# Kernel optimization log

Hardware: AMD Instinct MI355X
Metric: run time of the kernel (lower is better)

Reference implementation:

```python
import jax, jax.numpy as jnp
import numpy as np

D = 1024  # input_dim

def setup_inputs() -> dict:
    key = jax.random.key(0)
    ks = jax.random.split(key, 7)
    s = 1.0 / np.sqrt(D)
    x = jax.random.normal(ks[0], (8, 2048, D), dtype=jnp.float32)
    Wq = jax.random.uniform(ks[1], (D, D), jnp.float32, -s, s)
    bq = jax.random.uniform(ks[2], (D,), jnp.float32, -s, s)
    Wk = jax.random.uniform(ks[3], (D, D), jnp.float32, -s, s)
    bk = jax.random.uniform(ks[4], (D,), jnp.float32, -s, s)
    Wv = jax.random.uniform(ks[5], (D, D), jnp.float32, -s, s)
    bv = jax.random.uniform(ks[6], (D,), jnp.float32, -s, s)
    return {"x": x, "Wq": Wq, "bq": bq, "Wk": Wk, "bk": bk, "Wv": Wv, "bv": bv}

def reference(x, Wq, bq, Wk, bk, Wv, bv):
    # torch.nn.Linear: y = x @ W.T + b
    q = jnp.einsum('bsd,ed->bse', x, Wq) + bq
    k = jnp.einsum('bsd,ed->bse', x, Wk) + bk
    v = jnp.einsum('bsd,ed->bse', x, Wv) + bv
    scores = jnp.einsum('bqd,bkd->bqk', q, k) / jnp.sqrt(jnp.float32(x.shape[-1]))
    attn = jax.nn.softmax(scores, axis=2)
    return jnp.einsum('bqk,bkd->bqd', attn, v)
```

## Files before the change

### kernel.cpp

```cpp
#include <hip/hip_runtime.h>
#include <stdint.h>


typedef __bf16 bf16_t;
typedef __bf16 bf16x8 __attribute__((ext_vector_type(8)));
typedef __bf16 bf16x4 __attribute__((ext_vector_type(4)));
typedef float f32x4 __attribute__((ext_vector_type(4)));

__device__ __forceinline__ void gload_lds16(const bf16_t* g, bf16_t* l) {
    __builtin_amdgcn_global_load_lds((const __attribute__((address_space(1))) void*)g,
                                     (__attribute__((address_space(3))) void*)l,
                                     16, 0, 0);
}

template <int EPI, int LDA, int LDB>
__device__ __forceinline__ void gemm256_core(
    bf16_t* __restrict__ lds,
    const bf16_t* __restrict__ A,
    const bf16_t* __restrict__ B,
    bf16_t* __restrict__ Cb, float* __restrict__ Cf, int ldc,
    float* __restrict__ aux, float scale, int K,
    int m0, int n0)
{
    const int t    = threadIdx.x;
    const int lane = t & 63;
    const int wave = t >> 6;
    const int wm   = wave >> 2;
    const int wn   = wave & 3;
    const int lr   = lane & 15;
    const int quad = lane >> 4;

    const int rowS = t >> 2;
    const int qS   = (t & 3) ^ ((rowS >> 1) & 3);
    const bf16_t* Ag = A + (size_t)(m0 + rowS) * LDA + qS * 8;
    const bf16_t* Bg = B + (size_t)(n0 + rowS) * LDB + qS * 8;
    const int dst0 = t * 8;

    const int ko   = (quad ^ ((lr >> 1) & 3)) * 8;
    const int aoff = (wm * 128 + lr) * 32 + ko;
    const int boff = (wn * 64 + lr) * 32 + ko;

    f32x4 acc[8][4];
#pragma unroll
    for (int i = 0; i < 8; i++)
#pragma unroll
        for (int j = 0; j < 4; j++) acc[i][j] = (f32x4){0.f, 0.f, 0.f, 0.f};

    const int T = K >> 5;

#pragma unroll
    for (int tt = 0; tt < 3; ++tt) {
        bf16_t* Ab = lds + tt * 16384;
        bf16_t* Bb = Ab + 8192;
        const int kt = tt * 32;
        gload_lds16(Ag + kt,                     Ab + dst0);
        gload_lds16(Ag + kt + (size_t)128 * LDA, Ab + 4096 + dst0);
        gload_lds16(Bg + kt,                     Bb + dst0);
        gload_lds16(Bg + kt + (size_t)128 * LDB, Bb + 4096 + dst0);
    }
    asm volatile("s_waitcnt vmcnt(8)" ::: "memory");
    __builtin_amdgcn_s_barrier();
    __builtin_amdgcn_sched_barrier(0);

    for (int tk = 0; tk < T; ++tk) {
        const bf16_t* Ab = lds + (tk & 3) * 16384;
        const bf16_t* Bb = Ab + 8192;
        bf16x8 af[8], bfr[4];
#pragma unroll
        for (int j = 0; j < 4; ++j)
            bfr[j] = *(const bf16x8*)(Bb + boff + 512 * j);
#pragma unroll
        for (int i = 0; i < 8; ++i)
            af[i] = *(const bf16x8*)(Ab + aoff + 512 * i);
        __builtin_amdgcn_s_barrier();
        __builtin_amdgcn_sched_barrier(0);
        __builtin_amdgcn_s_setprio(1);
#pragma unroll
        for (int i = 0; i < 4; ++i)
#pragma unroll
            for (int j = 0; j < 4; ++j)
                acc[i][j] = __builtin_amdgcn_mfma_f32_16x16x32_bf16(af[i], bfr[j], acc[i][j], 0, 0, 0);
        __builtin_amdgcn_s_setprio(0);
        if (tk + 3 < T) {
            bf16_t* An = lds + ((tk + 3) & 3) * 16384;
            bf16_t* Bn = An + 8192;
            const int kt = (tk + 3) * 32;
            gload_lds16(Ag + kt,                     An + dst0);
            gload_lds16(Ag + kt + (size_t)128 * LDA, An + 4096 + dst0);
            gload_lds16(Bg + kt,                     Bn + dst0);
            gload_lds16(Bg + kt + (size_t)128 * LDB, Bn + 4096 + dst0);
            asm volatile("s_waitcnt vmcnt(8)" ::: "memory");
        } else if (tk + 2 < T) {
            asm volatile("s_waitcnt vmcnt(4)" ::: "memory");
        } else {
            asm volatile("s_waitcnt vmcnt(0)" ::: "memory");
        }
        __builtin_amdgcn_s_barrier();
        __builtin_amdgcn_sched_barrier(0);
        __builtin_amdgcn_s_setprio(1);
#pragma unroll
        for (int i = 4; i < 8; ++i)
#pragma unroll
            for (int j = 0; j < 4; ++j)
                acc[i][j] = __builtin_amdgcn_mfma_f32_16x16x32_bf16(af[i], bfr[j], acc[i][j], 0, 0, 0);
        __builtin_amdgcn_s_setprio(0);
    }

    if (EPI == 0 || EPI == 1) {
#pragma unroll
        for (int h = 0; h < 2; ++h) {
            __syncthreads();
            if (wm == h) {
#pragma unroll
                for (int j = 0; j < 4; ++j) {
                    const int col = wn * 64 + j * 16 + lr;
                    const float bv = (EPI == 0) ? aux[n0 + col] : 0.f;
#pragma unroll
                    for (int i = 0; i < 8; ++i) {
                        const int row = i * 16 + quad * 4;
#pragma unroll
                        for (int r = 0; r < 4; ++r) {
                            float v = (EPI == 0) ? (acc[i][j][r] + bv)
                                                 : __expf(acc[i][j][r] * scale);
                            lds[(row + r) * 264 + col] = (__bf16)v;
                        }
                    }
                }
            }
            __syncthreads();
            const int r2 = t >> 2;
            const int c0 = (t & 3) * 8;
            float part = 0.f;
#pragma unroll
            for (int c = 0; c < 8; ++c) {
                bf16x8 v = *(const bf16x8*)(lds + r2 * 264 + c0 + c * 32);
                *(bf16x8*)(Cb + (size_t)(m0 + h * 128 + r2) * ldc + n0 + c0 + c * 32) = v;
                if (EPI == 1) {
#pragma unroll
                    for (int e = 0; e < 8; ++e) part += (float)v[e];
                }
            }
            if (EPI == 1) {
                part += __shfl_xor(part, 1);
                part += __shfl_xor(part, 2);
                if ((t & 3) == 0) atomicAdd(aux + m0 + h * 128 + r2, part);
            }
        }
    } else if (EPI == 2) {
#pragma unroll
        for (int j = 0; j < 4; ++j) {
            const int col = n0 + wn * 64 + j * 16 + lr;
            const float s = 1.0f / aux[col];
            float* ccol = Cf + (size_t)col * ldc + m0 + wm * 128;
#pragma unroll
            for (int i = 0; i < 8; ++i) {
                f32x4 v = acc[i][j];
                v[0] *= s; v[1] *= s; v[2] *= s; v[3] *= s;
                *(f32x4*)(ccol + i * 16 + quad * 4) = v;
            }
        }
    } else {
#pragma unroll
        for (int j = 0; j < 4; ++j) {
            const int col = n0 + wn * 64 + j * 16 + lr;
            const float bv = aux[col];
#pragma unroll
            for (int i = 0; i < 8; ++i) {
                const int rowg = m0 + wm * 128 + i * 16 + quad * 4;
                const int b    = rowg >> 11;
                const int s    = rowg & 2047;
                bf16x4 p = { (__bf16)(acc[i][j][0] + bv), (__bf16)(acc[i][j][1] + bv),
                             (__bf16)(acc[i][j][2] + bv), (__bf16)(acc[i][j][3] + bv) };
                *(bf16x4*)(Cb + ((size_t)b << 21) + ((size_t)col << 11) + s) = p;
            }
        }
    }
}


__global__ __launch_bounds__(512, 1) void k_qkv3(
    const bf16_t* __restrict__ xb, const bf16_t* __restrict__ Wb,
    bf16_t* __restrict__ Q, bf16_t* __restrict__ Vt,
    const float* __restrict__ bq, const float* __restrict__ bk,
    const float* __restrict__ bv)
{
    __shared__ bf16_t lds[65536];
    const int lid  = blockIdx.x + 8 * blockIdx.y;
    const int xcd  = lid & 7;
    const int slot = lid >> 3;
    const int z    = slot >> 5;
    const int rem  = slot & 31;
    const int xt   = rem & 3;
    const int yt   = xcd * 8 + (rem >> 2);
    if (z < 2) {
        float* bias = (float*)((z == 0) ? bq : bk);
        gemm256_core<0, 1024, 1024>(lds, xb, Wb + (size_t)z * 1048576,
                                    Q + (size_t)z * 16777216, nullptr, 1024,
                                    bias, 0.f, 1024, yt * 256, xt * 256);
    } else {
        gemm256_core<3, 1024, 1024>(lds, xb, Wb + (size_t)2 * 1048576,
                                    Vt, nullptr, 0,
                                    (float*)bv, 0.f, 1024, yt * 256, xt * 256);
    }
}

__global__ __launch_bounds__(512, 1) void k_scores(
    const bf16_t* __restrict__ Q, const bf16_t* __restrict__ Km,
    bf16_t* __restrict__ U, float* __restrict__ l)
{
    __shared__ bf16_t lds[65536];
    const int lid = blockIdx.x + 8 * blockIdx.y;
    const int b   = lid & 7;
    const int si  = lid >> 3;
    const int xt  = si & 7;
    const int yt  = si >> 3;
    gemm256_core<1, 1024, 1024>(lds, Q + (size_t)b * 2048 * 1024,
                                Km + (size_t)b * 2048 * 1024,
                                U + (size_t)b * 2048 * 2048, nullptr, 2048,
                                l + b * 2048, 0.03125f, 1024,
                                yt * 256, xt * 256);
}

__global__ __launch_bounds__(512, 1) void k_pv(
    const bf16_t* __restrict__ U, const bf16_t* __restrict__ Vt,
    float* __restrict__ Out, float* __restrict__ l)
{
    __shared__ bf16_t lds[65536];
    const int lid = blockIdx.x + 8 * blockIdx.y;
    const int b   = lid & 7;
    const int si  = lid >> 3;
    const int xt  = si & 7;
    const int yt  = si >> 3;
    gemm256_core<2, 2048, 2048>(lds, Vt + ((size_t)b << 21),
                                U + (size_t)b * 2048 * 2048,
                                nullptr, Out + (size_t)b * 2048 * 1024, 1024,
                                l + b * 2048, 0.f, 2048,
                                yt * 256, xt * 256);
}

__global__ __launch_bounds__(256) void k_cvt(
    const float* __restrict__ in, bf16_t* __restrict__ out, long ngroups,
    float* __restrict__ l)
{
    long idx    = (long)blockIdx.x * blockDim.x + threadIdx.x;
    long stride = (long)gridDim.x * blockDim.x;
    if (blockIdx.x < 64) l[blockIdx.x * 256 + threadIdx.x] = 0.f;
    for (long i = idx; i < ngroups; i += stride) {
        float4 v = ((const float4*)in)[i];
        bf16x4 o = { (__bf16)v.x, (__bf16)v.y, (__bf16)v.z, (__bf16)v.w };
        ((bf16x4*)out)[i] = o;
    }
}

__global__ __launch_bounds__(256) void k_cvt3(
    const float* __restrict__ w0, const float* __restrict__ w1,
    const float* __restrict__ w2, bf16_t* __restrict__ out)
{
    const int z = blockIdx.z;
    const float* in = (z == 0) ? w0 : (z == 1) ? w1 : w2;
    bf16_t* o = out + (size_t)z * 1048576;
    long i = (long)blockIdx.x * blockDim.x + threadIdx.x;
    float4 v = ((const float4*)in)[i];
    bf16x4 ov = { (__bf16)v.x, (__bf16)v.y, (__bf16)v.z, (__bf16)v.w };
    ((bf16x4*)o)[i] = ov;
}


extern "C" void kernel_launch(void* const* d_in, const int* in_sizes, int n_in,
                              void* d_out, int out_size, void* d_ws, size_t ws_size,
                              hipStream_t stream)
{
    const float* x  = (const float*)d_in[0];
    const float* Wq = (const float*)d_in[1];
    const float* bq = (const float*)d_in[2];
    const float* Wk = (const float*)d_in[3];
    const float* bk = (const float*)d_in[4];
    const float* Wv = (const float*)d_in[5];
    const float* bv = (const float*)d_in[6];

    bf16_t* Q    = (bf16_t*)d_ws;
    bf16_t* Km   = Q + 16777216;
    bf16_t* Vt   = Km + 16777216;
    bf16_t* U    = Vt + 16777216;
    bf16_t* xb   = U;
    bf16_t* Wb   = U + 33554432;
    float*  l    = (float*)(Wb + 3145728);

    k_cvt<<<dim3(2048), 256, 0, stream>>>(x, xb, 16777216 / 4, l);
    k_cvt3<<<dim3(1024, 1, 3), 256, 0, stream>>>(Wq, Wk, Wv, Wb);
    k_qkv3<<<dim3(8, 96), 512, 0, stream>>>(xb, Wb, Q, Vt, bq, bk, bv);
    k_scores<<<dim3(8, 64), 512, 0, stream>>>(Q, Km, U, l);
    k_pv<<<dim3(8, 32), 512, 0, stream>>>(U, Vt, (float*)d_out, l);
}
```

Measured before the change: 380.7 us.

## Software-pipeline LDS fragment loads with MFMA in the GEMM main loop

Restructures the GEMM inner loop so that LDS fragment reads are interleaved with MFMA groups. The first half of the A fragments and the B fragments for the next k-tile are prefetched into registers while the current tile's MFMAs run, and the second half of A is loaded mid-iteration. The goal is to hide LDS read latency behind matrix math instead of stalling before each tile's compute. In exchange it raises register pressure, and the prefetch of the next buffer relies on the existing barrier and waitcnt ordering being sufficient.

```diff
diff --git a/kernel.cpp b/kernel.cpp
--- a/kernel.cpp
+++ b/kernel.cpp
@@ -62,24 +62,37 @@
     __builtin_amdgcn_s_barrier();
     __builtin_amdgcn_sched_barrier(0);
 
+    bf16x8 afA[4], bfA[4];
+#pragma unroll
+    for (int j = 0; j < 4; ++j)
+        bfA[j] = *(const bf16x8*)(lds + 8192 + boff + 512 * j);
+#pragma unroll
+    for (int i = 0; i < 4; ++i)
+        afA[i] = *(const bf16x8*)(lds + aoff + 512 * i);
+
     for (int tk = 0; tk < T; ++tk) {
         const bf16_t* Ab = lds + (tk & 3) * 16384;
-        const bf16_t* Bb = Ab + 8192;
-        bf16x8 af[8], bfr[4];
-#pragma unroll
-        for (int j = 0; j < 4; ++j)
-            bfr[j] = *(const bf16x8*)(Bb + boff + 512 * j);
-#pragma unroll
-        for (int i = 0; i < 8; ++i)
-            af[i] = *(const bf16x8*)(Ab + aoff + 512 * i);
         __builtin_amdgcn_s_barrier();
         __builtin_amdgcn_sched_barrier(0);
         __builtin_amdgcn_s_setprio(1);
 #pragma unroll
+        for (int i = 0; i < 2; ++i)
+#pragma unroll
+            for (int j = 0; j < 4; ++j)
+                acc[i][j] = __builtin_amdgcn_mfma_f32_16x16x32_bf16(afA[i], bfA[j], acc[i][j], 0, 0, 0);
+        __builtin_amdgcn_s_setprio(0);
+        __builtin_amdgcn_sched_barrier(0);
+        bf16x8 af2[4];
+#pragma unroll
         for (int i = 0; i < 4; ++i)
+            af2[i] = *(const bf16x8*)(Ab + aoff + 512 * (4 + i));
+        __builtin_amdgcn_sched_barrier(0);
+        __builtin_amdgcn_s_setprio(1);
+#pragma unroll
+        for (int i = 2; i < 4; ++i)
 #pragma unroll
             for (int j = 0; j < 4; ++j)
-                acc[i][j] = __builtin_amdgcn_mfma_f32_16x16x32_bf16(af[i], bfr[j], acc[i][j], 0, 0, 0);
+                acc[i][j] = __builtin_amdgcn_mfma_f32_16x16x32_bf16(afA[i], bfA[j], acc[i][j], 0, 0, 0);
         __builtin_amdgcn_s_setprio(0);
         if (tk + 3 < T) {
             bf16_t* An = lds + ((tk + 3) & 3) * 16384;
@@ -99,11 +112,31 @@
         __builtin_amdgcn_sched_barrier(0);
         __builtin_amdgcn_s_setprio(1);
 #pragma unroll
-        for (int i = 4; i < 8; ++i)
+        for (int i = 0; i < 2; ++i)
 #pragma unroll
             for (int j = 0; j < 4; ++j)
-                acc[i][j] = __builtin_amdgcn_mfma_f32_16x16x32_bf16(af[i], bfr[j], acc[i][j], 0, 0, 0);
+                acc[4 + i][j] = __builtin_amdgcn_mfma_f32_16x16x32_bf16(af2[i], bfA[j], acc[4 + i][j], 0, 0, 0);
         __builtin_amdgcn_s_setprio(0);
+        __builtin_amdgcn_sched_barrier(0);
+        const bf16_t* AbN = lds + (((tk + 1 < T) ? (tk + 1) : tk) & 3) * 16384;
+        const bf16_t* BbN = AbN + 8192;
+        bf16x8 naf[4], nbf[4];
+#pragma unroll
+        for (int j = 0; j < 4; ++j)
+            nbf[j] = *(const bf16x8*)(BbN + boff + 512 * j);
+#pragma unroll
+        for (int i = 0; i < 4; ++i)
+            naf[i] = *(const bf16x8*)(AbN + aoff + 512 * i);
+        __builtin_amdgcn_sched_barrier(0);
+        __builtin_amdgcn_s_setprio(1);
+#pragma unroll
+        for (int i = 2; i < 4; ++i)
+#pragma unroll
+            for (int j = 0; j < 4; ++j)
+                acc[4 + i][j] = __builtin_amdgcn_mfma_f32_16x16x32_bf16(af2[i], bfA[j], acc[4 + i][j], 0, 0, 0);
+        __builtin_amdgcn_s_setprio(0);
+#pragma unroll
+        for (int i = 0; i < 4; ++i) { afA[i] = naf[i]; bfA[i] = nbf[i]; }
     }
 
     if (EPI == 0 || EPI == 1) {
```

Measured after the change: 377.1 us. About the same (-0.9%).

## Switch GEMM mainloop to BK=64 double-buffered LDS with 8-way XOR swizzle

Applied to the files above, without the earlier changes.

Replaces the 4-stage, BK=32 LDS ring (with a split MFMA phase between barriers) by a 2-stage double buffer of 64-wide K tiles. Each iteration issues the next tile's global-to-LDS loads and then runs two K sub-steps of MFMAs, with one wait and barrier per 64-wide step. The swizzle moves from a 4-chunk XOR to an 8-chunk XOR on the row index to fit the wider rows. This halves the barrier count and raises the work per sync, but leaves fewer tiles in flight, so more global-load latency may be exposed.

```diff
diff --git a/kernel.cpp b/kernel.cpp
--- a/kernel.cpp
+++ b/kernel.cpp
@@ -22,23 +22,23 @@
     float* __restrict__ aux, float scale, int K,
     int m0, int n0)
 {
-    const int t    = threadIdx.x;
-    const int lane = t & 63;
-    const int wave = t >> 6;
+    const int th   = threadIdx.x;
+    const int lane = th & 63;
+    const int wave = th >> 6;
     const int wm   = wave >> 2;
     const int wn   = wave & 3;
     const int lr   = lane & 15;
     const int quad = lane >> 4;
-
-    const int rowS = t >> 2;
-    const int qS   = (t & 3) ^ ((rowS >> 1) & 3);
-    const bf16_t* Ag = A + (size_t)(m0 + rowS) * LDA + qS * 8;
-    const bf16_t* Bg = B + (size_t)(n0 + rowS) * LDB + qS * 8;
-    const int dst0 = t * 8;
-
-    const int ko   = (quad ^ ((lr >> 1) & 3)) * 8;
-    const int aoff = (wm * 128 + lr) * 32 + ko;
-    const int boff = (wn * 64 + lr) * 32 + ko;
+    const int lr7  = lr & 7;
+
+    const int rS = th >> 3;
+    const int cS = (th & 7) ^ (rS & 7);
+    const bf16_t* Ag = A + (size_t)(m0 + rS) * LDA + cS * 8;
+    const bf16_t* Bg = B + (size_t)(n0 + rS) * LDB + cS * 8;
+    const int dstS = th * 8;
+
+    const int arow = (wm * 128 + lr) * 64;
+    const int brow = (wn * 64 + lr) * 64;
 
     f32x4 acc[8][4];
 #pragma unroll
@@ -46,64 +46,47 @@
 #pragma unroll
         for (int j = 0; j < 4; j++) acc[i][j] = (f32x4){0.f, 0.f, 0.f, 0.f};
 
-    const int T = K >> 5;
-
-#pragma unroll
-    for (int tt = 0; tt < 3; ++tt) {
-        bf16_t* Ab = lds + tt * 16384;
-        bf16_t* Bb = Ab + 8192;
-        const int kt = tt * 32;
-        gload_lds16(Ag + kt,                     Ab + dst0);
-        gload_lds16(Ag + kt + (size_t)128 * LDA, Ab + 4096 + dst0);
-        gload_lds16(Bg + kt,                     Bb + dst0);
-        gload_lds16(Bg + kt + (size_t)128 * LDB, Bb + 4096 + dst0);
-    }
-    asm volatile("s_waitcnt vmcnt(8)" ::: "memory");
+    const int T = K >> 6;
+
+#pragma unroll
+    for (int l = 0; l < 4; ++l) {
+        gload_lds16(Ag + (size_t)(l * 64) * LDA, lds + l * 4096 + dstS);
+        gload_lds16(Bg + (size_t)(l * 64) * LDB, lds + 16384 + l * 4096 + dstS);
+    }
+    asm volatile("s_waitcnt vmcnt(0)" ::: "memory");
     __builtin_amdgcn_s_barrier();
-    __builtin_amdgcn_sched_barrier(0);
 
     for (int tk = 0; tk < T; ++tk) {
-        const bf16_t* Ab = lds + (tk & 3) * 16384;
-        const bf16_t* Bb = Ab + 8192;
-        bf16x8 af[8], bfr[4];
-#pragma unroll
-        for (int j = 0; j < 4; ++j)
-            bfr[j] = *(const bf16x8*)(Bb + boff + 512 * j);
-#pragma unroll
-        for (int i = 0; i < 8; ++i)
-            af[i] = *(const bf16x8*)(Ab + aoff + 512 * i);
+        bf16_t* cur = lds + (tk & 1) * 32768;
+        bf16_t* oth = lds + ((tk + 1) & 1) * 32768;
+        if (tk + 1 < T) {
+            const int kt = (tk + 1) * 64;
+#pragma unroll
+            for (int l = 0; l < 4; ++l) {
+                gload_lds16(Ag + kt + (size_t)(l * 64) * LDA, oth + l * 4096 + dstS);
+                gload_lds16(Bg + kt + (size_t)(l * 64) * LDB, oth + 16384 + l * 4096 + dstS);
+            }
+        }
+#pragma unroll
+        for (int kk = 0; kk < 2; ++kk) {
+            const int ko = ((kk * 4 + quad) ^ lr7) * 8;
+            bf16x8 af[8], bfr[4];
+#pragma unroll
+            for (int j = 0; j < 4; ++j)
+                bfr[j] = *(const bf16x8*)(cur + 16384 + brow + j * 1024 + ko);
+#pragma unroll
+            for (int i = 0; i < 8; ++i)
+                af[i] = *(const bf16x8*)(cur + arow + i * 1024 + ko);
+            __builtin_amdgcn_s_setprio(1);
+#pragma unroll
+            for (int i = 0; i < 8; ++i)
+#pragma unroll
+                for (int j = 0; j < 4; ++j)
+                    acc[i][j] = __builtin_amdgcn_mfma_f32_16x16x32_bf16(af[i], bfr[j], acc[i][j], 0, 0, 0);
+            __builtin_amdgcn_s_setprio(0);
+        }
+        asm volatile("s_waitcnt vmcnt(0)" ::: "memory");
         __builtin_amdgcn_s_barrier();
-        __builtin_amdgcn_sched_barrier(0);
-        __builtin_amdgcn_s_setprio(1);
-#pragma unroll
-        for (int i = 0; i < 4; ++i)
-#pragma unroll
-            for (int j = 0; j < 4; ++j)
-                acc[i][j] = __builtin_amdgcn_mfma_f32_16x16x32_bf16(af[i], bfr[j], acc[i][j], 0, 0, 0);
-        __builtin_amdgcn_s_setprio(0);
-        if (tk + 3 < T) {
-            bf16_t* An = lds + ((tk + 3) & 3) * 16384;
-            bf16_t* Bn = An + 8192;
-            const int kt = (tk + 3) * 32;
-            gload_lds16(Ag + kt,                     An + dst0);
-            gload_lds16(Ag + kt + (size_t)128 * LDA, An + 4096 + dst0);
-            gload_lds16(Bg + kt,                     Bn + dst0);
-            gload_lds16(Bg + kt + (size_t)128 * LDB, Bn + 4096 + dst0);
-            asm volatile("s_waitcnt vmcnt(8)" ::: "memory");
-        } else if (tk + 2 < T) {
-            asm volatile("s_waitcnt vmcnt(4)" ::: "memory");
-        } else {
-            asm volatile("s_waitcnt vmcnt(0)" ::: "memory");
-        }
-        __builtin_amdgcn_s_barrier();
-        __builtin_amdgcn_sched_barrier(0);
-        __builtin_amdgcn_s_setprio(1);
-#pragma unroll
-        for (int i = 4; i < 8; ++i)
-#pragma unroll
-            for (int j = 0; j < 4; ++j)
-                acc[i][j] = __builtin_amdgcn_mfma_f32_16x16x32_bf16(af[i], bfr[j], acc[i][j], 0, 0, 0);
-        __builtin_amdgcn_s_setprio(0);
     }
 
     if (EPI == 0 || EPI == 1) {
@@ -128,8 +111,8 @@
                 }
             }
             __syncthreads();
-            const int r2 = t >> 2;
-            const int c0 = (t & 3) * 8;
+            const int r2 = th >> 2;
+            const int c0 = (th & 3) * 8;
             float part = 0.f;
 #pragma unroll
             for (int c = 0; c < 8; ++c) {
@@ -143,7 +126,7 @@
             if (EPI == 1) {
                 part += __shfl_xor(part, 1);
                 part += __shfl_xor(part, 2);
-                if ((t & 3) == 0) atomicAdd(aux + m0 + h * 128 + r2, part);
+                if ((th & 3) == 0) atomicAdd(aux + m0 + h * 128 + r2, part);
             }
         }
     } else if (EPI == 2) {
```

Measured after the change: 369.7 us. 2.9% less time.
